# Performance work log

Measured on AMD Instinct MI355X. Metric: run time of the kernel, lower is better.

Reference implementation:

```python
import jax, jax.numpy as jnp
import numpy as np

B, O, C, HID, H, W = 4, 8, 256, 128, 64, 64
STEPS = 2  # message passing steps


def _conv3x3(x, w, b):
    # x: [N,Cin,H,W], w: [Cout,Cin,3,3]
    y = jax.lax.conv_general_dilated(x, w, window_strides=(1, 1), padding='SAME',
                                     dimension_numbers=('NCHW', 'OIHW', 'NCHW'))
    return y + b[None, :, None, None]


def setup_inputs() -> dict:
    key = jax.random.key(0)
    ks = jax.random.split(key, 6)
    return {
        'batch_node_feats': jax.random.normal(ks[0], (B, C, H, W), jnp.float32),
        'batch_previous_masks': jax.random.uniform(ks[1], (B, O, H, W), jnp.float32),
        'batch_valid_indices': jnp.ones((B, O), jnp.bool_),
        'batch_previous_states': jnp.zeros((B, O), jnp.float32),  # unused (use_temporal_features=False)
        'enc_w': jax.random.normal(ks[2], (HID, C + 1, 3, 3), jnp.float32) * 0.02,
        'enc_b': jnp.zeros((HID,), jnp.float32),
        'gcn_w': jax.random.normal(ks[3], (HID, 2 * HID, 3, 3), jnp.float32) * 0.02,
        'gcn_b': jnp.zeros((HID,), jnp.float32),
        'ro_w': jax.random.normal(ks[4], (1, C + HID, 3, 3), jnp.float32) * 0.02,
        'ro_b': jnp.zeros((1,), jnp.float32),
    }


def reference(batch_node_feats, batch_previous_masks, batch_valid_indices,
              batch_previous_states, enc_w, enc_b, gcn_w, gcn_b, ro_w, ro_b):
    # All objects valid (batch_valid_indices all True) -> fully vectorized over B and O.
    feats = jnp.broadcast_to(batch_node_feats[:, None], (B, O, C, H, W))
    # Mask encoder: per-object state from frame feats + previous object mask.
    enc_in = jnp.concatenate([feats, batch_previous_masks[:, :, None]], axis=2)
    states = jax.nn.relu(_conv3x3(enc_in.reshape(B * O, C + 1, H, W), enc_w, enc_b))
    states = states.reshape(B, O, HID, H, W)
    # Fully-connected message passing: neighbors of i = all objects except i.
    for _ in range(STEPS):
        agg = states.sum(axis=1, keepdims=True) - states  # sum over others
        gcn_in = jnp.concatenate([states, agg], axis=2).reshape(B * O, 2 * HID, H, W)
        states = jax.nn.relu(_conv3x3(gcn_in, gcn_w, gcn_b)).reshape(B, O, HID, H, W)
    # Readout: per-object mask logits -> sigmoid.
    ro_in = jnp.concatenate([feats, states], axis=2).reshape(B * O, C + HID, H, W)
    out_masks = jax.nn.sigmoid(_conv3x3(ro_in, ro_w, ro_b)).reshape(B, O, H, W)
    return out_masks  # out_states is None when use_temporal_features=False
```

## Files before the change

### kernel.cpp

```cpp
#include <hip/hip_runtime.h>
#include <math.h>


typedef unsigned short ushort_t;
typedef _Float16 f16x8 __attribute__((ext_vector_type(8)));
typedef float f32x4 __attribute__((ext_vector_type(4)));

#define GLDS(gsrc, ldst)                                                      \
    __builtin_amdgcn_global_load_lds(                                         \
        (const __attribute__((address_space(1))) unsigned int*)(gsrc),        \
        (__attribute__((address_space(3))) unsigned int*)(ldst), 16, 0, 0)

__device__ __forceinline__ ushort_t f2h(float f) {
    _Float16 h = (_Float16)f;
    return *(ushort_t*)&h;
}
__device__ __forceinline__ float h2f(ushort_t u) {
    _Float16 h = *(_Float16*)&u;
    return (float)h;
}

__global__ __launch_bounds__(256) void prep_all(
    const float* __restrict__ feats, const float* __restrict__ enc_w,
    const float* __restrict__ gcn_w, const float* __restrict__ ro_w,
    ushort_t* __restrict__ featsT, ushort_t* __restrict__ WencF,
    ushort_t* __restrict__ WgcnS, ushort_t* __restrict__ WgcnD,
    ushort_t* __restrict__ WroQ, ushort_t* __restrict__ WroS)
{
    __shared__ float tile[64][65];
    int bid = blockIdx.x, t = threadIdx.x;
    if (bid < 1024) {
        int pt = bid & 63, ct = (bid >> 6) & 3, img = bid >> 8;
        int px_l = t & 63;
        const float* src = feats + ((size_t)img * 256 + ct * 64) * 4096 + pt * 64;
#pragma unroll
        for (int j = 0; j < 16; ++j) {
            int ci_l = (t >> 6) + j * 4;
            tile[px_l][ci_l] = src[(size_t)ci_l * 4096 + px_l];
        }
        __syncthreads();
        int px = t >> 2;
#pragma unroll
        for (int j = 0; j < 2; ++j) {
            int c8 = ((t & 3) + j * 4) * 8;
            uint4 v; ushort_t* pv = (ushort_t*)&v;
#pragma unroll
            for (int k = 0; k < 8; ++k) pv[k] = f2h(tile[px][c8 + k]);
            int cc = ct * 2 + (c8 >> 5);
            *(uint4*)(featsT + ((size_t)img * 8 + cc) * 131072 +
                      (size_t)(pt * 64 + px) * 32 + (c8 & 31)) = v;
        }
        return;
    }
    int i = (bid - 1024) * 256 + t;
    if (i < 294912) {
        int ci32 = i & 31, co = (i >> 5) & 127, tc = i >> 12;
        int tt = tc >> 3, cc = tc & 7, ci = cc * 32 + ci32;
        WencF[i] = f2h(enc_w[(co * 257 + ci) * 9 + tt]);
    } else if (i < 442368) {
        int j = i - 294912;
        int ci32 = j & 31, co = (j >> 5) & 127, tc = j >> 12;
        int tt = tc >> 2, cc = tc & 3, ci = cc * 32 + ci32;
        WgcnS[j] = f2h(gcn_w[(co * 256 + 128 + ci) * 9 + tt]);
    } else if (i < 589824) {
        int j = i - 442368;
        int ci32 = j & 31, co = (j >> 5) & 127, tc = j >> 12;
        int tt = tc >> 2, cc = tc & 3, ci = cc * 32 + ci32;
        WgcnD[j] = f2h(gcn_w[(co * 256 + ci) * 9 + tt] -
                       gcn_w[(co * 256 + 128 + ci) * 9 + tt]);
    } else if (i < 592128) {
        int j = i - 589824;
        int k = j & 7, r = j >> 3;
        int tt = r % 9, cq = r / 9, q = cq & 3, cc = cq >> 2;
        WroQ[j] = f2h(ro_w[(cc * 32 + q * 8 + k) * 9 + tt]);
    } else if (i < 593280) {
        int j = i - 592128;
        int k = j & 7, r = j >> 3;
        int tt = r % 9, cq = r / 9, q = cq & 3, cc = cq >> 2;
        WroS[j] = f2h(ro_w[(256 + cc * 32 + q * 8 + k) * 9 + tt]);
    }
}

template<int NCCBLK, bool FUSE, bool SUMIN>
__global__ __launch_bounds__(256, 3) void conv_k(
    const ushort_t* __restrict__ x, const ushort_t* __restrict__ W,
    ushort_t* __restrict__ out,
    const ushort_t* __restrict__ addp, const float* __restrict__ bias,
    int ncc_img)
{
    __shared__ ushort_t raw[25088];
    ushort_t* xs = raw;
    ushort_t* wlds = raw + 16896;
    ushort_t* eb16 = raw;

    const int rp = blockIdx.x, img = blockIdx.y, kz = blockIdx.z;
    const int row0 = rp * 2;
    const int cc0 = kz * NCCBLK;
    const int nchunk = 9 * NCCBLK;
    const int tid = threadIdx.x;
    const int w = tid >> 6, lane = tid & 63, lq = lane >> 4, lr = lane & 15;
    const int cg = w >> 1, pg = w & 1;

    const size_t objstride = (size_t)ncc_img * 131072;
    const ushort_t* xb = SUMIN ? x + (size_t)img * 8 * objstride
                               : x + (size_t)img * objstride;
    const int aoff0 = (cg * 64 + lr) * 32 + lq * 8;

    if (tid < 64) {
        int b = tid >> 5, r = (tid >> 3) & 3, c = (tid >> 2) & 1, s = tid & 3;
        *(uint4*)(xs + b * 8448 + r * 2112 + (c ? 65 : 0) * 32 + s * 8) =
            make_uint4(0, 0, 0, 0);
    }

    f32x4 acc[4][4];
#pragma unroll
    for (int a = 0; a < 4; ++a)
#pragma unroll
        for (int p = 0; p < 4; ++p) acc[a][p] = (f32x4){0.f, 0.f, 0.f, 0.f};

    const int gy = row0 - 1 + w;
    const bool row_ok = (unsigned)gy < 64u;
#define STAGE_ACT(cc_, buf_)                                                    \
    {                                                                           \
        ushort_t* dst = xs + (buf_) * 8448 + w * 2112 + 32;                     \
        if (row_ok) {                                                           \
            const ushort_t* src = xb + (size_t)(cc_) * 131072 + (size_t)gy * 2048; \
            if constexpr (SUMIN) {                                              \
                _Pragma("unroll")                                               \
                for (int u_ = 0; u_ < 4; ++u_) {                                \
                    f16x8 a_ = {0, 0, 0, 0, 0, 0, 0, 0};                        \
                    _Pragma("unroll")                                           \
                    for (int o_ = 0; o_ < 8; ++o_)                              \
                        a_ = a_ + *(const f16x8*)(src + (size_t)o_ * objstride + \
                                                  u_ * 512 + lane * 8);         \
                    *(f16x8*)(dst + u_ * 512 + lane * 8) = a_;                  \
                }                                                               \
            } else {                                                            \
                GLDS(src + 0 * 512 + lane * 8, dst + 0 * 512);                  \
                GLDS(src + 1 * 512 + lane * 8, dst + 1 * 512);                  \
                GLDS(src + 2 * 512 + lane * 8, dst + 2 * 512);                  \
                GLDS(src + 3 * 512 + lane * 8, dst + 3 * 512);                  \
            }                                                                   \
        } else {                                                                \
            *(uint4*)(dst + 0 * 512 + lane * 8) = make_uint4(0, 0, 0, 0);       \
            *(uint4*)(dst + 1 * 512 + lane * 8) = make_uint4(0, 0, 0, 0);       \
            *(uint4*)(dst + 2 * 512 + lane * 8) = make_uint4(0, 0, 0, 0);       \
            *(uint4*)(dst + 3 * 512 + lane * 8) = make_uint4(0, 0, 0, 0);       \
        }                                                                       \
    }
#define STAGE_W(t_, cc_, buf_)                                                  \
    {                                                                           \
        const ushort_t* src = W + ((size_t)((t_) * ncc_img + (cc_)) * 4096);    \
        ushort_t* dst = wlds + (buf_) * 4096;                                   \
        GLDS(src + (w * 2 + 0) * 512 + lane * 8, dst + (w * 2 + 0) * 512);      \
        GLDS(src + (w * 2 + 1) * 512 + lane * 8, dst + (w * 2 + 1) * 512);      \
    }

    STAGE_ACT(cc0, 0);
    STAGE_W(0, cc0, 0);

    int kc = 0;
#pragma unroll
    for (int ccl = 0; ccl < NCCBLK; ++ccl) {
        const int cc = cc0 + ccl;
        const int xbuf = ccl & 1;
#pragma unroll
        for (int t = 0; t < 9; ++t, ++kc) {
            __syncthreads();
            if (kc + 1 < nchunk) {
                if (t == 8) {
                    STAGE_W(0, cc + 1, (kc + 1) & 1);
                    STAGE_ACT(cc + 1, (ccl + 1) & 1);
                } else {
                    STAGE_W(t + 1, cc, (kc + 1) & 1);
                }
            }
            const int dy = t / 3, dx = t - 3 * dy;
            const ushort_t* wl = wlds + (kc & 1) * 4096 + aoff0;
            const ushort_t* xl = xs + xbuf * 8448 + (pg + dy) * 2112 + (dx + lr) * 32 + lq * 8;
            f16x8 A0 = *(const f16x8*)(wl);
            f16x8 A1 = *(const f16x8*)(wl + 512);
            f16x8 A2 = *(const f16x8*)(wl + 1024);
            f16x8 A3 = *(const f16x8*)(wl + 1536);
#pragma unroll
            for (int p = 0; p < 4; ++p) {
                f16x8 Bf = *(const f16x8*)(xl + p * 512);
                acc[0][p] = __builtin_amdgcn_mfma_f32_16x16x32_f16(A0, Bf, acc[0][p], 0, 0, 0);
                acc[1][p] = __builtin_amdgcn_mfma_f32_16x16x32_f16(A1, Bf, acc[1][p], 0, 0, 0);
                acc[2][p] = __builtin_amdgcn_mfma_f32_16x16x32_f16(A2, Bf, acc[2][p], 0, 0, 0);
                acc[3][p] = __builtin_amdgcn_mfma_f32_16x16x32_f16(A3, Bf, acc[3][p], 0, 0, 0);
            }
        }
    }

    ushort_t* obase = out + (size_t)(kz * gridDim.y + img) * 524288;
    const int b4 = img >> 3;
#pragma unroll
    for (int r = 0; r < 2; ++r) {
        __syncthreads();
        if (pg == r) {
#pragma unroll
            for (int cf = 0; cf < 4; ++cf)
#pragma unroll
                for (int pf = 0; pf < 4; ++pf) {
                    int px = pf * 16 + lr;
                    int co_l = cg * 64 + cf * 16 + lq * 4;
                    ushort_t pk[4];
#pragma unroll
                    for (int j = 0; j < 4; ++j) pk[j] = f2h(acc[cf][pf][j]);
                    *(uint2*)(eb16 + px * 136 + co_l) = *(uint2*)pk;
                }
        }
        __syncthreads();
#pragma unroll
        for (int k2 = 0; k2 < 4; ++k2) {
            int i = tid + k2 * 256;
            int px = i >> 4, c16 = i & 15;
            int pxg = (row0 + r) * 64 + px;
            size_t coff = (size_t)(c16 >> 2) * 131072 + (size_t)pxg * 32 + (c16 & 3) * 8;
            uint4 v = *(uint4*)(eb16 + px * 136 + c16 * 8);
            if constexpr (FUSE) {
                const ushort_t* vp = (const ushort_t*)&v;
                float vv[8];
#pragma unroll
                for (int k = 0; k < 8; ++k) vv[k] = h2f(vp[k]) + bias[c16 * 8 + k];
#pragma unroll
                for (int p = 0; p < 4; ++p) {
                    uint4 av = *(const uint4*)(addp + (size_t)(p * 4 + b4) * 524288 + coff);
                    const ushort_t* ap = (const ushort_t*)&av;
#pragma unroll
                    for (int k = 0; k < 8; ++k) vv[k] += h2f(ap[k]);
                }
                uint4 sv; ushort_t* sp = (ushort_t*)&sv;
#pragma unroll
                for (int k = 0; k < 8; ++k) sp[k] = f2h(fmaxf(vv[k], 0.f));
                *(uint4*)(obase + coff) = sv;
            } else {
                *(uint4*)(obase + coff) = v;
            }
        }
    }
#undef STAGE_ACT
#undef STAGE_W
}

__global__ __launch_bounds__(256) void enc_obj_ro(
    const float* __restrict__ masks, const float* __restrict__ enc_w,
    const float* __restrict__ enc_b, const ushort_t* __restrict__ U1p,
    const ushort_t* __restrict__ featsT, const ushort_t* __restrict__ WroQ,
    ushort_t* __restrict__ S, ushort_t* __restrict__ USum,
    float* __restrict__ YR)
{
    int bid = blockIdx.x, tid = threadIdx.x;
    if (bid >= 1024) {
        int i = (bid - 1024) * 256 + tid;
        int cu = i & 31, px = (i >> 5) & 4095, b = i >> 17;
        int cc = cu >> 2, q = cu & 3;
        int y = px >> 6, xcol = px & 63;
        const ushort_t* wp = WroQ + (size_t)(cc * 4 + q) * 72;
        float wreg[9][8];
#pragma unroll
        for (int t = 0; t < 9; ++t) {
            uint4 wv = *(const uint4*)(wp + t * 8);
            const ushort_t* wq = (const ushort_t*)&wv;
#pragma unroll
            for (int k = 0; k < 8; ++k) wreg[t][k] = h2f(wq[k]);
        }
        const ushort_t* fb = featsT + (size_t)(b * 8 + cc) * 131072 + q * 8;
        float acc = 0.f;
#pragma unroll
        for (int dy = 0; dy < 3; ++dy) {
            int gy = y + dy - 1;
            if ((unsigned)gy >= 64u) continue;
#pragma unroll
            for (int dx = 0; dx < 3; ++dx) {
                int gx = xcol + dx - 1;
                if ((unsigned)gx >= 64u) continue;
                uint4 v = *(const uint4*)(fb + (size_t)(gy * 64 + gx) * 32);
                const ushort_t* vp = (const ushort_t*)&v;
#pragma unroll
                for (int k = 0; k < 8; ++k)
                    acc = fmaf(h2f(vp[k]), wreg[dy * 3 + dx][k], acc);
            }
        }
#pragma unroll
        for (int d = 16; d >= 1; d >>= 1) acc += __shfl_down(acc, d, 32);
        if (cu == 0) YR[b * 4096 + px] = acc;
        return;
    }
    int i = bid * 256 + tid;
    int s = i & 3, px = (i >> 2) & 4095, cc = (i >> 14) & 3, b = i >> 16;
    int co = cc * 32 + s * 8;
    int y = px >> 6, xx = px & 63;
    size_t coff = (size_t)cc * 131072 + (size_t)px * 32 + s * 8;
    float base[8];
#pragma unroll
    for (int k = 0; k < 8; ++k) base[k] = enc_b[co + k];
#pragma unroll
    for (int p = 0; p < 4; ++p) {
        uint4 v = *(const uint4*)(U1p + (size_t)(p * 4 + b) * 524288 + coff);
        const ushort_t* vp = (const ushort_t*)&v;
#pragma unroll
        for (int k = 0; k < 8; ++k) base[k] += h2f(vp[k]);
    }
    float wm[8][9];
#pragma unroll
    for (int k = 0; k < 8; ++k) {
        const float* wp = enc_w + (size_t)((co + k) * 257 + 256) * 9;
#pragma unroll
        for (int t = 0; t < 9; ++t) wm[k][t] = wp[t];
    }
    float sacc[8] = {0, 0, 0, 0, 0, 0, 0, 0};
#pragma unroll
    for (int o = 0; o < 8; ++o) {
        const float* m = masks + (size_t)(b * 8 + o) * 4096;
        float mt[9];
#pragma unroll
        for (int dy = 0; dy < 3; ++dy)
#pragma unroll
            for (int dx = 0; dx < 3; ++dx) {
                int gy_ = y + dy - 1, gx = xx + dx - 1;
                mt[dy * 3 + dx] =
                    ((unsigned)gy_ < 64u && (unsigned)gx < 64u) ? m[gy_ * 64 + gx] : 0.f;
            }
        uint4 sv; ushort_t* sp = (ushort_t*)&sv;
#pragma unroll
        for (int k = 0; k < 8; ++k) {
            float acc = base[k];
#pragma unroll
            for (int t = 0; t < 9; ++t) acc = fmaf(mt[t], wm[k][t], acc);
            acc = fmaxf(acc, 0.f);
            sacc[k] += acc;
            sp[k] = f2h(acc);
        }
        *(uint4*)(S + (size_t)(b * 8 + o) * 524288 + coff) = sv;
    }
    uint4 sv; ushort_t* sp = (ushort_t*)&sv;
#pragma unroll
    for (int k = 0; k < 8; ++k) sp[k] = f2h(sacc[k]);
    *(uint4*)(USum + (size_t)b * 524288 + coff) = sv;
}

__global__ __launch_bounds__(256) void ro_obj(
    const ushort_t* __restrict__ S, const ushort_t* __restrict__ WroS,
    const float* __restrict__ ro_b, const float* __restrict__ YR,
    float* __restrict__ out)
{
    int i = blockIdx.x * 256 + threadIdx.x;
    int cu = i & 15, px = (i >> 4) & 4095, n = i >> 16;
    int b = n >> 3;
    int cc = cu >> 2, q = cu & 3;
    int y = px >> 6, xcol = px & 63;
    const ushort_t* wp = WroS + (size_t)(cc * 4 + q) * 72;
    float wreg[9][8];
#pragma unroll
    for (int t = 0; t < 9; ++t) {
        uint4 wv = *(const uint4*)(wp + t * 8);
        const ushort_t* wq = (const ushort_t*)&wv;
#pragma unroll
        for (int k = 0; k < 8; ++k) wreg[t][k] = h2f(wq[k]);
    }
    const ushort_t* sb = S + ((size_t)n * 4 + cc) * 131072 + q * 8;
    float acc = 0.f;
#pragma unroll
    for (int dy = 0; dy < 3; ++dy) {
        int gy = y + dy - 1;
        if ((unsigned)gy >= 64u) continue;
#pragma unroll
        for (int dx = 0; dx < 3; ++dx) {
            int gx = xcol + dx - 1;
            if ((unsigned)gx >= 64u) continue;
            uint4 v = *(const uint4*)(sb + (size_t)(gy * 64 + gx) * 32);
            const ushort_t* vp = (const ushort_t*)&v;
#pragma unroll
            for (int k = 0; k < 8; ++k)
                acc = fmaf(h2f(vp[k]), wreg[dy * 3 + dx][k], acc);
        }
    }
#pragma unroll
    for (int d = 8; d >= 1; d >>= 1) acc += __shfl_down(acc, d, 16);
    if (cu == 0) {
        float v = acc + YR[b * 4096 + px] + ro_b[0];
        out[n * 4096 + px] = 1.f / (1.f + __expf(-v));
    }
}

extern "C" void kernel_launch(void* const* d_in, const int* in_sizes, int n_in,
                              void* d_out, int out_size, void* d_ws, size_t ws_size,
                              hipStream_t stream)
{
    const float* feats = (const float*)d_in[0];
    const float* masks = (const float*)d_in[1];
    const float* enc_w = (const float*)d_in[4];
    const float* enc_b = (const float*)d_in[5];
    const float* gcn_w = (const float*)d_in[6];
    const float* gcn_b = (const float*)d_in[7];
    const float* ro_w  = (const float*)d_in[8];
    const float* ro_b  = (const float*)d_in[9];
    float* out = (float*)d_out;

    ushort_t* WencF  = (ushort_t*)d_ws;
    ushort_t* WgcnS  = WencF + 294912;
    ushort_t* WgcnD  = WgcnS + 147456;
    ushort_t* WroQ   = WgcnD + 147456;
    ushort_t* WroS   = WroQ + 2304;
    ushort_t* featsT = WroS + 1152;
    ushort_t* Sa     = featsT + 4194304;
    ushort_t* Sb     = Sa + 16777216;
    ushort_t* USum   = Sb + 16777216;
    ushort_t* U1p16  = USum + 2097152;
    ushort_t* U2p16  = U1p16 + 8388608;
    float*    YR     = (float*)(U2p16 + 8388608);

    dim3 blk(256);

    prep_all<<<3344, blk, 0, stream>>>(feats, enc_w, gcn_w, ro_w,
                                       featsT, WencF, WgcnS, WgcnD, WroQ, WroS);

    conv_k<2, false, false><<<dim3(32, 4, 4), blk, 0, stream>>>(
        featsT, WencF, U1p16, nullptr, nullptr, 8);
    enc_obj_ro<<<3072, blk, 0, stream>>>(masks, enc_w, enc_b, U1p16,
                                         featsT, WroQ, Sa, USum, YR);

    conv_k<1, false, false><<<dim3(32, 4, 4), blk, 0, stream>>>(
        USum, WgcnS, U2p16, nullptr, nullptr, 4);
    conv_k<4, true, false><<<dim3(32, 32, 1), blk, 0, stream>>>(
        Sa, WgcnD, Sb, U2p16, gcn_b, 4);

    conv_k<1, false, true><<<dim3(32, 4, 4), blk, 0, stream>>>(
        Sb, WgcnS, U2p16, nullptr, nullptr, 4);
    conv_k<4, true, false><<<dim3(32, 32, 1), blk, 0, stream>>>(
        Sb, WgcnD, Sa, U2p16, gcn_b, 4);

    ro_obj<<<8192, blk, 0, stream>>>(Sa, WroS, ro_b, YR, out);
}
```

Baseline: 274.8 us.

## Load conv weights straight into double-buffered registers and cut per-tap barriers

The conv kernel no longer stages weight tiles through LDS. Each wave now loads its A fragments directly from global memory into two register sets, prefetching the next tap's weights while the current tap runs. Activations are still staged in LDS, but only once per channel chunk, so there is one barrier per chunk instead of one per tap, and the LDS footprint shrinks. In exchange, waves that share a channel group fetch the same weights twice from cache, register pressure rises, and global load latency is exposed more directly.

```diff
diff --git a/kernel.cpp b/kernel.cpp
--- a/kernel.cpp
+++ b/kernel.cpp
@@ -88,9 +88,8 @@
     const ushort_t* __restrict__ addp, const float* __restrict__ bias,
     int ncc_img)
 {
-    __shared__ ushort_t raw[25088];
+    __shared__ ushort_t raw[16896];
     ushort_t* xs = raw;
-    ushort_t* wlds = raw + 16896;
     ushort_t* eb16 = raw;
 
     const int rp = blockIdx.x, img = blockIdx.y, kz = blockIdx.z;
@@ -104,7 +103,7 @@
     const size_t objstride = (size_t)ncc_img * 131072;
     const ushort_t* xb = SUMIN ? x + (size_t)img * 8 * objstride
                                : x + (size_t)img * objstride;
-    const int aoff0 = (cg * 64 + lr) * 32 + lq * 8;
+    const ushort_t* wgb = W + (size_t)(cg * 64 + lr) * 32 + lq * 8;
 
     if (tid < 64) {
         int b = tid >> 5, r = (tid >> 3) & 3, c = (tid >> 2) & 1, s = tid & 3;
@@ -148,40 +147,40 @@
             *(uint4*)(dst + 3 * 512 + lane * 8) = make_uint4(0, 0, 0, 0);       \
         }                                                                       \
     }
-#define STAGE_W(t_, cc_, buf_)                                                  \
-    {                                                                           \
-        const ushort_t* src = W + ((size_t)((t_) * ncc_img + (cc_)) * 4096);    \
-        ushort_t* dst = wlds + (buf_) * 4096;                                   \
-        GLDS(src + (w * 2 + 0) * 512 + lane * 8, dst + (w * 2 + 0) * 512);      \
-        GLDS(src + (w * 2 + 1) * 512 + lane * 8, dst + (w * 2 + 1) * 512);      \
-    }
-
+#define WLOAD(dst_, t_, cc_)                                                    \
+    do {                                                                        \
+        const ushort_t* p_ = wgb + (size_t)((t_) * ncc_img + (cc_)) * 4096;     \
+        dst_[0] = *(const f16x8*)(p_);                                          \
+        dst_[1] = *(const f16x8*)(p_ + 512);                                    \
+        dst_[2] = *(const f16x8*)(p_ + 1024);                                   \
+        dst_[3] = *(const f16x8*)(p_ + 1536);                                   \
+    } while (0)
+
+    f16x8 wr0[4], wr1[4];
     STAGE_ACT(cc0, 0);
-    STAGE_W(0, cc0, 0);
+    WLOAD(wr0, 0, cc0);
 
     int kc = 0;
 #pragma unroll
     for (int ccl = 0; ccl < NCCBLK; ++ccl) {
         const int cc = cc0 + ccl;
         const int xbuf = ccl & 1;
+        __syncthreads();
+        if (ccl + 1 < NCCBLK) STAGE_ACT(cc + 1, xbuf ^ 1);
 #pragma unroll
         for (int t = 0; t < 9; ++t, ++kc) {
-            __syncthreads();
             if (kc + 1 < nchunk) {
-                if (t == 8) {
-                    STAGE_W(0, cc + 1, (kc + 1) & 1);
-                    STAGE_ACT(cc + 1, (ccl + 1) & 1);
-                } else {
-                    STAGE_W(t + 1, cc, (kc + 1) & 1);
-                }
+                const int nt = (t == 8) ? 0 : t + 1;
+                const int nc = (t == 8) ? cc + 1 : cc;
+                if ((kc & 1) == 0) { WLOAD(wr1, nt, nc); }
+                else               { WLOAD(wr0, nt, nc); }
             }
+            const f16x8 A0 = ((kc & 1) == 0) ? wr0[0] : wr1[0];
+            const f16x8 A1 = ((kc & 1) == 0) ? wr0[1] : wr1[1];
+            const f16x8 A2 = ((kc & 1) == 0) ? wr0[2] : wr1[2];
+            const f16x8 A3 = ((kc & 1) == 0) ? wr0[3] : wr1[3];
             const int dy = t / 3, dx = t - 3 * dy;
-            const ushort_t* wl = wlds + (kc & 1) * 4096 + aoff0;
             const ushort_t* xl = xs + xbuf * 8448 + (pg + dy) * 2112 + (dx + lr) * 32 + lq * 8;
-            f16x8 A0 = *(const f16x8*)(wl);
-            f16x8 A1 = *(const f16x8*)(wl + 512);
-            f16x8 A2 = *(const f16x8*)(wl + 1024);
-            f16x8 A3 = *(const f16x8*)(wl + 1536);
 #pragma unroll
             for (int p = 0; p < 4; ++p) {
                 f16x8 Bf = *(const f16x8*)(xl + p * 512);
@@ -241,7 +240,7 @@
         }
     }
 #undef STAGE_ACT
-#undef STAGE_W
+#undef WLOAD
 }
 
 __global__ __launch_bounds__(256) void enc_obj_ro(
```

New measurement: 300.2 us. +9.2%, slower.
